# Kernel optimization log

Hardware: AMD Instinct MI355X
Metric: run time of the kernel (lower is better)

Reference implementation:

```python
import jax, jax.numpy as jnp
import numpy as np

DIM = 512
LEAF_DIM = 128
DEPTH = 3
NUM_LEAVES = 2 ** DEPTH  # 8
B, T = 4, 2048


def setup_inputs() -> dict:
    key = jax.random.key(0)
    ks = jax.random.split(key, 16)
    sD = DIM ** -0.5
    sF = LEAF_DIM ** -0.5
    inp = {
        "inputs": jax.random.normal(ks[0], (B, T, DIM), jnp.float32),
        "training": 1,
    }
    # per-level node (routing) params: (D, 2^d)
    for d in range(DEPTH):
        n = 2 ** d
        inp[f"wn{d}"] = jax.random.normal(ks[1 + d], (DIM, n), jnp.float32) * sD
        inp[f"bn{d}"] = jnp.zeros((n,), jnp.float32)
    # stacked leaf FFN params
    inp["w1a"] = jax.random.normal(ks[8], (NUM_LEAVES, DIM, LEAF_DIM), jnp.float32) * sD
    inp["b1a"] = jnp.zeros((NUM_LEAVES, LEAF_DIM), jnp.float32)
    inp["w1b"] = jax.random.normal(ks[9], (NUM_LEAVES, DIM, LEAF_DIM), jnp.float32) * sD
    inp["b1b"] = jnp.zeros((NUM_LEAVES, LEAF_DIM), jnp.float32)
    inp["w2"] = jax.random.normal(ks[10], (NUM_LEAVES, LEAF_DIM, DIM), jnp.float32) * sF
    inp["b2"] = jnp.zeros((NUM_LEAVES, DIM), jnp.float32)
    return inp


def reference(inputs, training, wn0, bn0, wn1, bn1, wn2, bn2, w1a, b1a, w1b, b1b, w2, b2):
    Bs, Ts, D = inputs.shape
    L = NUM_LEAVES
    sg = jax.lax.stop_gradient
    mixture = jnp.ones((Bs, Ts, L), inputs.dtype)
    for wn, bn in ((wn0, bn0), (wn1, bn1), (wn2, bn2)):
        n = wn.shape[1]  # nodes at this depth
        c = jax.nn.sigmoid(inputs @ wn + bn)  # (B,T,n)
        if training:
            # straight-through hard rounding
            c = c - sg(c) + sg(jnp.rint(c))
        else:
            c = jnp.rint(c)
        c_nc = jnp.stack([c, 1.0 - c], -1).reshape(Bs, Ts, 2 * n, 1)
        mixture = (mixture.reshape(Bs, Ts, 2 * n, L // (2 * n)) * c_nc)
    mixture = mixture.reshape(Bs, Ts, L)
    # dense per-leaf gated FFN, masked by mixture
    h = (jnp.einsum('btd,ldf->btlf', inputs, w1a) + b1a) * \
        (jnp.einsum('btd,ldf->btlf', inputs, w1b) + b1b)  # (B,T,L,F)
    y2 = jnp.einsum('btlf,lfd->btld', h, w2) + b2          # (B,T,L,D)
    y = (y2 * mixture[..., None]).sum(-2)                  # (B,T,D)
    return y
```

## Files before the change

### kernel.cpp

```cpp
#include <hip/hip_runtime.h>
#include <hip/hip_bf16.h>

#define N_TOK 8192
#define DIM   512
#define FDIM  128
#define BM    16

typedef __attribute__((ext_vector_type(8))) short short8;
typedef __attribute__((ext_vector_type(4))) float floatx4;

__device__ inline short f2bf(float f) {
    union { float f; unsigned u; } v; v.f = f;
    unsigned r = (v.u + 0x7FFF + ((v.u >> 16) & 1)) >> 16;
    return (short)r;
}

__global__ __launch_bounds__(256) void k_prep(
    const float* __restrict__ x,
    const float* __restrict__ wn0, const float* __restrict__ bn0,
    const float* __restrict__ wn1, const float* __restrict__ bn1,
    const float* __restrict__ wn2, const float* __restrict__ bn2,
    const float* __restrict__ w1a, const float* __restrict__ w1b,
    const float* __restrict__ w2,
    int* __restrict__ counts, int* __restrict__ lists,
    short* __restrict__ pw1a, short* __restrict__ pw1b, short* __restrict__ pw2)
{
    const int blk = blockIdx.x;
    if (blk < 128) {
        __shared__ int leafs[64];
        const int t = threadIdx.x;
        const int wave = t >> 6, lane = t & 63;
        const int d0 = lane * 8;
        float v0[8], v1[16], v2[32];
        #pragma unroll
        for (int j = 0; j < 8; ++j)  v0[j] = wn0[d0 + j];
        #pragma unroll
        for (int j = 0; j < 16; ++j) v1[j] = wn1[d0 * 2 + j];
        #pragma unroll
        for (int j = 0; j < 32; ++j) v2[j] = wn2[d0 * 4 + j];
        const float b0s = bn0[0];
        const float b1s[2] = {bn1[0], bn1[1]};
        const float b2s[4] = {bn2[0], bn2[1], bn2[2], bn2[3]};
        for (int i = 0; i < 16; ++i) {
            const int tok = blk * 64 + wave * 16 + i;
            const float4* xp = (const float4*)(x + tok * DIM + d0);
            const float4 xa = xp[0], xb = xp[1];
            const float xv[8] = {xa.x, xa.y, xa.z, xa.w, xb.x, xb.y, xb.z, xb.w};
            float a0 = 0.f, a1[2] = {0.f, 0.f}, a2[4] = {0.f, 0.f, 0.f, 0.f};
            #pragma unroll
            for (int j = 0; j < 8; ++j) {
                a0    += xv[j] * v0[j];
                a1[0] += xv[j] * v1[j * 2];     a1[1] += xv[j] * v1[j * 2 + 1];
                a2[0] += xv[j] * v2[j * 4];     a2[1] += xv[j] * v2[j * 4 + 1];
                a2[2] += xv[j] * v2[j * 4 + 2]; a2[3] += xv[j] * v2[j * 4 + 3];
            }
            #pragma unroll
            for (int off = 32; off >= 1; off >>= 1) {
                a0    += __shfl_xor(a0, off, 64);
                a1[0] += __shfl_xor(a1[0], off, 64);
                a1[1] += __shfl_xor(a1[1], off, 64);
                a2[0] += __shfl_xor(a2[0], off, 64);
                a2[1] += __shfl_xor(a2[1], off, 64);
                a2[2] += __shfl_xor(a2[2], off, 64);
                a2[3] += __shfl_xor(a2[3], off, 64);
            }
            int p = (a0 + b0s > 0.f) ? 0 : 1;
            const float t1 = a1[p] + b1s[p];
            p = p * 2 + ((t1 > 0.f) ? 0 : 1);
            const float t2 = a2[p] + b2s[p];
            p = p * 2 + ((t2 > 0.f) ? 0 : 1);
            if (lane == 0) leafs[wave * 16 + i] = p;
        }
        __syncthreads();
        if (t < 8) {
            const int l = t;
            int c = 0;
            for (int i = 0; i < 64; ++i) c += (leafs[i] == l);
            if (c > 0) {
                int base = atomicAdd(counts + l * 16, c);
                int j = 0;
                for (int i = 0; i < 64; ++i)
                    if (leafs[i] == l) lists[l * N_TOK + base + (j++)] = blk * 64 + i;
            }
        }
    } else {
        const int wid  = (blk - 128) * 4 + (threadIdx.x >> 6);
        const int lane = threadIdx.x & 63;
        const int q = lane >> 4, m = lane & 15;
        if (wid < 2048) {
            const float* src = (wid < 1024) ? w1a : w1b;
            short*       dst = (wid < 1024) ? pw1a : pw1b;
            const int f = wid & 1023;
            const int l = f >> 7, kb = (f >> 3) & 15, nt = f & 7;
            const float* s = src + l * 65536 + (kb * 32 + q * 8) * FDIM + nt * 16 + m;
            short8 o;
            #pragma unroll
            for (int j = 0; j < 8; ++j) o[j] = f2bf(s[j * FDIM]);
            *(short8*)(dst + f * 512 + lane * 8) = o;
        } else {
            const int f = wid - 2048;
            const int l = f >> 7, kb = (f >> 5) & 3, nt = f & 31;
            const float* s = w2 + l * 65536 + (kb * 32 + q * 8) * DIM + nt * 16 + m;
            short8 o;
            #pragma unroll
            for (int j = 0; j < 8; ++j) o[j] = f2bf(s[j * DIM]);
            *(short8*)(pw2 + f * 512 + lane * 8) = o;
        }
    }
}

__global__ __launch_bounds__(256) void k_ffn(
    const float* __restrict__ x,
    const float* __restrict__ b1a, const float* __restrict__ b1b,
    const float* __restrict__ b2,
    const short* __restrict__ pw1a, const short* __restrict__ pw1b,
    const short* __restrict__ pw2,
    const int* __restrict__ counts, const int* __restrict__ lists,
    float* __restrict__ out)
{
    const int leaf = blockIdx.y;
    const int tile = blockIdx.x;
    const int cnt  = counts[leaf * 16];
    if (tile * BM >= cnt) return;

    __shared__ int   toks[BM];
    __shared__ short xs[BM][DIM + 8];
    __shared__ short hs[BM][FDIM + 8];

    const int t = threadIdx.x;
    if (t < BM) {
        const int idx = tile * BM + t;
        toks[t] = lists[leaf * N_TOK + ((idx < cnt) ? idx : cnt - 1)];
    }
    __syncthreads();

    {
        const int row = t >> 4, c0 = (t & 15) * 32;
        const float4* src = (const float4*)(x + toks[row] * DIM + c0);
        #pragma unroll
        for (int u = 0; u < 4; ++u) {
            const float4 fa = src[u * 2], fb = src[u * 2 + 1];
            short8 o;
            o[0] = f2bf(fa.x); o[1] = f2bf(fa.y); o[2] = f2bf(fa.z); o[3] = f2bf(fa.w);
            o[4] = f2bf(fb.x); o[5] = f2bf(fb.y); o[6] = f2bf(fb.z); o[7] = f2bf(fb.w);
            *(short8*)&xs[row][c0 + u * 8] = o;
        }
    }
    __syncthreads();

    const int wave = t >> 6, lane = t & 63;
    const int qd = lane >> 4, mm = lane & 15;

    floatx4 accA0 = {0,0,0,0}, accA1 = {0,0,0,0}, accB0 = {0,0,0,0}, accB1 = {0,0,0,0};
    const int nt0 = wave * 2, nt1 = wave * 2 + 1;
    #pragma unroll
    for (int kb = 0; kb < 16; ++kb) {
        const short8 af  = *(const short8*)&xs[mm][kb * 32 + qd * 8];
        const short8 ba0 = *(const short8*)(pw1a + (((leaf * 16 + kb) * 8 + nt0) * 512) + lane * 8);
        const short8 ba1 = *(const short8*)(pw1a + (((leaf * 16 + kb) * 8 + nt1) * 512) + lane * 8);
        const short8 bb0 = *(const short8*)(pw1b + (((leaf * 16 + kb) * 8 + nt0) * 512) + lane * 8);
        const short8 bb1 = *(const short8*)(pw1b + (((leaf * 16 + kb) * 8 + nt1) * 512) + lane * 8);
        accA0 = __builtin_amdgcn_mfma_f32_16x16x32_bf16(af, ba0, accA0, 0, 0, 0);
        accA1 = __builtin_amdgcn_mfma_f32_16x16x32_bf16(af, ba1, accA1, 0, 0, 0);
        accB0 = __builtin_amdgcn_mfma_f32_16x16x32_bf16(af, bb0, accB0, 0, 0, 0);
        accB1 = __builtin_amdgcn_mfma_f32_16x16x32_bf16(af, bb1, accB1, 0, 0, 0);
    }
    {
        const int c0 = nt0 * 16 + mm, c1 = nt1 * 16 + mm;
        const float ba0 = b1a[leaf * FDIM + c0], ba1 = b1a[leaf * FDIM + c1];
        const float bb0 = b1b[leaf * FDIM + c0], bb1 = b1b[leaf * FDIM + c1];
        #pragma unroll
        for (int r = 0; r < 4; ++r) {
            const int row = qd * 4 + r;
            hs[row][c0] = f2bf((accA0[r] + ba0) * (accB0[r] + bb0));
            hs[row][c1] = f2bf((accA1[r] + ba1) * (accB1[r] + bb1));
        }
    }
    __syncthreads();

    floatx4 acc[8];
    #pragma unroll
    for (int j = 0; j < 8; ++j) acc[j] = (floatx4){0, 0, 0, 0};
    #pragma unroll
    for (int kb = 0; kb < 4; ++kb) {
        const short8 af = *(const short8*)&hs[mm][kb * 32 + qd * 8];
        #pragma unroll
        for (int j = 0; j < 8; ++j) {
            const int nt = wave * 8 + j;
            const short8 bf = *(const short8*)(pw2 + (((leaf * 4 + kb) * 32 + nt) * 512) + lane * 8);
            acc[j] = __builtin_amdgcn_mfma_f32_16x16x32_bf16(af, bf, acc[j], 0, 0, 0);
        }
    }
    const int rem = cnt - tile * BM;
    #pragma unroll
    for (int j = 0; j < 8; ++j) {
        const int col = (wave * 8 + j) * 16 + mm;
        const float bias = b2[leaf * DIM + col];
        #pragma unroll
        for (int r = 0; r < 4; ++r) {
            const int row = qd * 4 + r;
            if (row < rem) out[toks[row] * DIM + col] = acc[j][r] + bias;
        }
    }
}

extern "C" void kernel_launch(void* const* d_in, const int* in_sizes, int n_in,
                              void* d_out, int out_size, void* d_ws, size_t ws_size,
                              hipStream_t stream) {
    const float* x   = (const float*)d_in[0];
    const float* wn0 = (const float*)d_in[2];
    const float* bn0 = (const float*)d_in[3];
    const float* wn1 = (const float*)d_in[4];
    const float* bn1 = (const float*)d_in[5];
    const float* wn2 = (const float*)d_in[6];
    const float* bn2 = (const float*)d_in[7];
    const float* w1a = (const float*)d_in[8];
    const float* b1a = (const float*)d_in[9];
    const float* w1b = (const float*)d_in[10];
    const float* b1b = (const float*)d_in[11];
    const float* w2  = (const float*)d_in[12];
    const float* b2  = (const float*)d_in[13];
    float* out = (float*)d_out;

    char* ws = (char*)d_ws;
    int*   counts = (int*)(ws);
    int*   lists  = (int*)(ws + 512);
    short* pw1a   = (short*)(ws + 262656);
    short* pw1b   = (short*)(ws + 262656 + 1048576);
    short* pw2    = (short*)(ws + 262656 + 2097152);

    hipMemsetAsync(counts, 0, 512, stream);
    k_prep<<<896, 256, 0, stream>>>(x, wn0, bn0, wn1, bn1, wn2, bn2,
                                    w1a, w1b, w2, counts, lists, pw1a, pw1b, pw2);
    k_ffn<<<dim3(512, 8), 256, 0, stream>>>(x, b1a, b1b, b2, pw1a, pw1b, pw2,
                                            counts, lists, out);
}
```

Measured before the change: 135.0 us.

## Double FFN token tile to 32 rows and pre-convert inputs to bf16

Each FFN block now handles 32 routed tokens with 512 threads (8 waves). Every wave loads one weight fragment and reuses it across two 16-row MFMA tiles, which halves weight fetches per token in both GEMMs. The prep kernel also writes a bf16 copy of the inputs to workspace, so the gather in the FFN kernel reads half the bytes and skips the per-block fp32-to-bf16 conversion. The costs are an extra global write in prep, more wasted rows in partially filled tiles, and a tighter register budget from the (512, 4) launch bounds.

```diff
diff --git a/kernel.cpp b/kernel.cpp
--- a/kernel.cpp
+++ b/kernel.cpp
@@ -4,7 +4,7 @@
 #define N_TOK 8192
 #define DIM   512
 #define FDIM  128
-#define BM    16
+#define BM    32
 
 typedef __attribute__((ext_vector_type(8))) short short8;
 typedef __attribute__((ext_vector_type(4))) float floatx4;
@@ -23,7 +23,8 @@
     const float* __restrict__ w1a, const float* __restrict__ w1b,
     const float* __restrict__ w2,
     int* __restrict__ counts, int* __restrict__ lists,
-    short* __restrict__ pw1a, short* __restrict__ pw1b, short* __restrict__ pw2)
+    short* __restrict__ pw1a, short* __restrict__ pw1b, short* __restrict__ pw2,
+    short* __restrict__ xbf)
 {
     const int blk = blockIdx.x;
     if (blk < 128) {
@@ -46,6 +47,10 @@
             const float4* xp = (const float4*)(x + tok * DIM + d0);
             const float4 xa = xp[0], xb = xp[1];
             const float xv[8] = {xa.x, xa.y, xa.z, xa.w, xb.x, xb.y, xb.z, xb.w};
+            short8 xo;
+            #pragma unroll
+            for (int j = 0; j < 8; ++j) xo[j] = f2bf(xv[j]);
+            *(short8*)(xbf + (size_t)tok * DIM + d0) = xo;
             float a0 = 0.f, a1[2] = {0.f, 0.f}, a2[4] = {0.f, 0.f, 0.f, 0.f};
             #pragma unroll
             for (int j = 0; j < 8; ++j) {
@@ -109,8 +114,8 @@
     }
 }
 
-__global__ __launch_bounds__(256) void k_ffn(
-    const float* __restrict__ x,
+__global__ __launch_bounds__(512, 4) void k_ffn(
+    const short* __restrict__ xbf,
     const float* __restrict__ b1a, const float* __restrict__ b1b,
     const float* __restrict__ b2,
     const short* __restrict__ pw1a, const short* __restrict__ pw1b,
@@ -136,44 +141,39 @@
 
     {
         const int row = t >> 4, c0 = (t & 15) * 32;
-        const float4* src = (const float4*)(x + toks[row] * DIM + c0);
-        #pragma unroll
-        for (int u = 0; u < 4; ++u) {
-            const float4 fa = src[u * 2], fb = src[u * 2 + 1];
-            short8 o;
-            o[0] = f2bf(fa.x); o[1] = f2bf(fa.y); o[2] = f2bf(fa.z); o[3] = f2bf(fa.w);
-            o[4] = f2bf(fb.x); o[5] = f2bf(fb.y); o[6] = f2bf(fb.z); o[7] = f2bf(fb.w);
-            *(short8*)&xs[row][c0 + u * 8] = o;
-        }
+        const short8* src = (const short8*)(xbf + (size_t)toks[row] * DIM + c0);
+        const short8 s0 = src[0], s1 = src[1], s2 = src[2], s3 = src[3];
+        short8* dst = (short8*)&xs[row][c0];
+        dst[0] = s0; dst[1] = s1; dst[2] = s2; dst[3] = s3;
     }
     __syncthreads();
 
     const int wave = t >> 6, lane = t & 63;
     const int qd = lane >> 4, mm = lane & 15;
 
-    floatx4 accA0 = {0,0,0,0}, accA1 = {0,0,0,0}, accB0 = {0,0,0,0}, accB1 = {0,0,0,0};
-    const int nt0 = wave * 2, nt1 = wave * 2 + 1;
+    floatx4 aA0 = {0,0,0,0}, aA1 = {0,0,0,0}, aB0 = {0,0,0,0}, aB1 = {0,0,0,0};
+    const short* pa = pw1a + ((leaf * 16) * 8 + wave) * 512 + lane * 8;
+    const short* pb = pw1b + ((leaf * 16) * 8 + wave) * 512 + lane * 8;
     #pragma unroll
     for (int kb = 0; kb < 16; ++kb) {
-        const short8 af  = *(const short8*)&xs[mm][kb * 32 + qd * 8];
-        const short8 ba0 = *(const short8*)(pw1a + (((leaf * 16 + kb) * 8 + nt0) * 512) + lane * 8);
-        const short8 ba1 = *(const short8*)(pw1a + (((leaf * 16 + kb) * 8 + nt1) * 512) + lane * 8);
-        const short8 bb0 = *(const short8*)(pw1b + (((leaf * 16 + kb) * 8 + nt0) * 512) + lane * 8);
-        const short8 bb1 = *(const short8*)(pw1b + (((leaf * 16 + kb) * 8 + nt1) * 512) + lane * 8);
-        accA0 = __builtin_amdgcn_mfma_f32_16x16x32_bf16(af, ba0, accA0, 0, 0, 0);
-        accA1 = __builtin_amdgcn_mfma_f32_16x16x32_bf16(af, ba1, accA1, 0, 0, 0);
-        accB0 = __builtin_amdgcn_mfma_f32_16x16x32_bf16(af, bb0, accB0, 0, 0, 0);
-        accB1 = __builtin_amdgcn_mfma_f32_16x16x32_bf16(af, bb1, accB1, 0, 0, 0);
+        const short8 af0 = *(const short8*)&xs[mm][kb * 32 + qd * 8];
+        const short8 af1 = *(const short8*)&xs[16 + mm][kb * 32 + qd * 8];
+        const short8 ba  = *(const short8*)(pa + kb * (8 * 512));
+        const short8 bb  = *(const short8*)(pb + kb * (8 * 512));
+        aA0 = __builtin_amdgcn_mfma_f32_16x16x32_bf16(af0, ba, aA0, 0, 0, 0);
+        aA1 = __builtin_amdgcn_mfma_f32_16x16x32_bf16(af1, ba, aA1, 0, 0, 0);
+        aB0 = __builtin_amdgcn_mfma_f32_16x16x32_bf16(af0, bb, aB0, 0, 0, 0);
+        aB1 = __builtin_amdgcn_mfma_f32_16x16x32_bf16(af1, bb, aB1, 0, 0, 0);
     }
     {
-        const int c0 = nt0 * 16 + mm, c1 = nt1 * 16 + mm;
-        const float ba0 = b1a[leaf * FDIM + c0], ba1 = b1a[leaf * FDIM + c1];
-        const float bb0 = b1b[leaf * FDIM + c0], bb1 = b1b[leaf * FDIM + c1];
+        const int c0 = wave * 16 + mm;
+        const float ba_ = b1a[leaf * FDIM + c0];
+        const float bb_ = b1b[leaf * FDIM + c0];
         #pragma unroll
         for (int r = 0; r < 4; ++r) {
-            const int row = qd * 4 + r;
-            hs[row][c0] = f2bf((accA0[r] + ba0) * (accB0[r] + bb0));
-            hs[row][c1] = f2bf((accA1[r] + ba1) * (accB1[r] + bb1));
+            const int r0 = qd * 4 + r;
+            hs[r0][c0]      = f2bf((aA0[r] + ba_) * (aB0[r] + bb_));
+            hs[16 + r0][c0] = f2bf((aA1[r] + ba_) * (aB1[r] + bb_));
         }
     }
     __syncthreads();
@@ -183,23 +183,26 @@
     for (int j = 0; j < 8; ++j) acc[j] = (floatx4){0, 0, 0, 0};
     #pragma unroll
     for (int kb = 0; kb < 4; ++kb) {
-        const short8 af = *(const short8*)&hs[mm][kb * 32 + qd * 8];
-        #pragma unroll
-        for (int j = 0; j < 8; ++j) {
-            const int nt = wave * 8 + j;
+        const short8 af0 = *(const short8*)&hs[mm][kb * 32 + qd * 8];
+        const short8 af1 = *(const short8*)&hs[16 + mm][kb * 32 + qd * 8];
+        #pragma unroll
+        for (int j = 0; j < 4; ++j) {
+            const int nt = wave * 4 + j;
             const short8 bf = *(const short8*)(pw2 + (((leaf * 4 + kb) * 32 + nt) * 512) + lane * 8);
-            acc[j] = __builtin_amdgcn_mfma_f32_16x16x32_bf16(af, bf, acc[j], 0, 0, 0);
+            acc[j * 2]     = __builtin_amdgcn_mfma_f32_16x16x32_bf16(af0, bf, acc[j * 2],     0, 0, 0);
+            acc[j * 2 + 1] = __builtin_amdgcn_mfma_f32_16x16x32_bf16(af1, bf, acc[j * 2 + 1], 0, 0, 0);
         }
     }
     const int rem = cnt - tile * BM;
     #pragma unroll
-    for (int j = 0; j < 8; ++j) {
-        const int col = (wave * 8 + j) * 16 + mm;
+    for (int j = 0; j < 4; ++j) {
+        const int col = (wave * 4 + j) * 16 + mm;
         const float bias = b2[leaf * DIM + col];
         #pragma unroll
         for (int r = 0; r < 4; ++r) {
-            const int row = qd * 4 + r;
-            if (row < rem) out[toks[row] * DIM + col] = acc[j][r] + bias;
+            const int r0 = qd * 4 + r;
+            if (r0 < rem)      out[toks[r0] * DIM + col]      = acc[j * 2][r]     + bias;
+            if (16 + r0 < rem) out[toks[16 + r0] * DIM + col] = acc[j * 2 + 1][r] + bias;
         }
     }
 }
@@ -228,10 +231,11 @@
     short* pw1a   = (short*)(ws + 262656);
     short* pw1b   = (short*)(ws + 262656 + 1048576);
     short* pw2    = (short*)(ws + 262656 + 2097152);
+    short* xbf    = (short*)(ws + 262656 + 3145728);
 
     hipMemsetAsync(counts, 0, 512, stream);
     k_prep<<<896, 256, 0, stream>>>(x, wn0, bn0, wn1, bn1, wn2, bn2,
-                                    w1a, w1b, w2, counts, lists, pw1a, pw1b, pw2);
-    k_ffn<<<dim3(512, 8), 256, 0, stream>>>(x, b1a, b1b, b2, pw1a, pw1b, pw2,
+                                    w1a, w1b, w2, counts, lists, pw1a, pw1b, pw2, xbf);
+    k_ffn<<<dim3(256, 8), 512, 0, stream>>>(xbf, b1a, b1b, b2, pw1a, pw1b, pw2,
                                             counts, lists, out);
 }
```

New measurement: 135.7 us. Within noise of the previous version (+0.5%).
